# Optimization experiments

Measured on AMD Instinct MI355X. Metric: run time of the kernel, lower is better.

The kernel has to match this reference:

```python
import jax, jax.numpy as jnp
import numpy as np

DIM = 384
HEADS = 8
HD = DIM // HEADS          # 48
RES = 7
N = RES * RES              # 49
B = 2048
SCALE = HD ** (-0.5)
EPS = 1e-12                # torch F.normalize default eps


def setup_inputs() -> dict:
    key = jax.random.key(0)
    ks = jax.random.split(key, 16)
    w = lambda k, shape: jax.random.normal(k, shape, jnp.float32) * 0.02
    return {
        "x": jax.random.normal(ks[0], (B, RES, RES, DIM), jnp.float32),
        # 1x1 convs stored as [out_ch, in_ch]
        "Wq": w(ks[1], (DIM, DIM)), "bq": w(ks[2], (DIM,)),
        "Wk": w(ks[3], (DIM, DIM)), "bk": w(ks[4], (DIM,)),
        "Wv": w(ks[5], (DIM, DIM)), "bv": w(ks[6], (DIM,)),
        # depthwise 3x3 conv, HWIO layout with feature_group_count=DIM -> [3,3,1,DIM]
        "Wvl": w(ks[7], (3, 3, 1, DIM)), "bvl": w(ks[8], (DIM,)),
        # talking-head 1x1 convs over the head axis: [out_heads, in_heads]
        "Wth1": w(ks[9], (HEADS, HEADS)), "bth1": w(ks[10], (HEADS,)),
        "Wth2": w(ks[11], (HEADS, HEADS)), "bth2": w(ks[12], (HEADS,)),
        "Wp": w(ks[13], (DIM, DIM)), "bp": w(ks[14], (DIM,)),
    }


def _conv1x1(x, W, b):
    # x: [B,H,W,C]; W: [O,C]
    return jnp.einsum('bhwc,oc->bhwo', x, W) + b


def _split_heads(y):
    # [B,H,W,DIM] -> [B, heads, head_dim, N]
    b = y.shape[0]
    return y.reshape(b, N, HEADS, HD).transpose(0, 2, 3, 1)


def _l2norm(t):
    # normalize over last axis (spatial N), matching F.normalize(dim=-1)
    n = jnp.sqrt(jnp.sum(t * t, axis=-1, keepdims=True))
    return t / jnp.maximum(n, EPS)


def reference(x, Wq, bq, Wk, bk, Wv, bv, Wvl, bvl,
              Wth1, bth1, Wth2, bth2, Wp, bp):
    # x: [B, H, W, C] (module internally permutes to NCHW; we stay NHWC)
    Bc, H, W_, C = x.shape
    q = _l2norm(_split_heads(_conv1x1(x, Wq, bq)))   # [B,h,c,N]
    k = _l2norm(_split_heads(_conv1x1(x, Wk, bk)))   # [B,h,c,N]
    v_map = _conv1x1(x, Wv, bv)                      # [B,H,W,DIM]
    v_local = jax.lax.conv_general_dilated(
        v_map, Wvl, window_strides=(1, 1), padding='SAME',
        dimension_numbers=('NHWC', 'HWIO', 'NHWC'),
        feature_group_count=DIM) + bvl               # depthwise 3x3
    v = _split_heads(v_map)                          # [B,h,c,N]

    # channel-channel attention: [B, heads, c, c]
    attn = jnp.einsum('bhcn,bhdn->bhcd', q, k) * SCALE
    attn = jnp.einsum('bhcd,gh->bgcd', attn, Wth1) + bth1[None, :, None, None]
    attn = jax.nn.softmax(attn, axis=-1)
    attn = jnp.einsum('bhcd,gh->bgcd', attn, Wth2) + bth2[None, :, None, None]

    o = jnp.einsum('bhcd,bhdn->bhcn', attn, v)       # [B,h,c,N]
    o = o.transpose(0, 3, 1, 2).reshape(Bc, H, W_, DIM) + v_local
    o = _conv1x1(jax.nn.relu(o), Wp, bp)
    return o
```

## Files before the change

kernel.cpp:

```cpp
#include <hip/hip_runtime.h>
#include <hip/hip_bf16.h>


typedef __attribute__((ext_vector_type(8))) short short8;
typedef __attribute__((ext_vector_type(4))) short short4v;
typedef __attribute__((ext_vector_type(4))) float f32x4;

#define NPOS   49
#define DIMC   384
#define SCALE_QK 0.14433756729740643f

#define REGA 0
#define REGB 38416
#define WOFF 36864
#define LDS_BYTES 76832

#define WBLK 159744

__device__ __forceinline__ unsigned short f2bf(float f) {
  __hip_bfloat16 h = __float2bfloat16(f);
  unsigned short u;
  __builtin_memcpy(&u, &h, 2);
  return u;
}
__device__ __forceinline__ float bf2f(unsigned short u) {
  union { unsigned u; float f; } v; v.u = ((unsigned)u) << 16;
  return v.f;
}

__global__ void wconv_kernel(const float* __restrict__ Wq, const float* __restrict__ Wk,
                             const float* __restrict__ Wv, const float* __restrict__ Wp,
                             const float* __restrict__ bq, const float* __restrict__ bk,
                             const float* __restrict__ bv, const float* __restrict__ bp,
                             unsigned short* __restrict__ dst) {
  int t = blockIdx.x * 256 + threadIdx.x;
  if (t >= 79872) return;
  int l = t & 63;
  int u = t >> 6;
  int ks = u % 13; u /= 13;
  int nt = u % 24;
  int g  = u / 24;
  const float* W  = (g == 0) ? Wq : (g == 1) ? Wk : (g == 2) ? Wv : Wp;
  const float* bb = (g == 0) ? bq : (g == 1) ? bk : (g == 2) ? bv : bp;
  int row = nt * 16 + (l & 15);
  short8 o8 = {0,0,0,0,0,0,0,0};
  if (ks < 12) {
    const float* sp = W + row * 384 + ks * 32 + (l >> 4) * 8;
    #pragma unroll
    for (int j = 0; j < 8; ++j) o8[j] = (short)f2bf(sp[j]);
  } else if ((l >> 4) == 0) {
    o8[0] = (short)f2bf(bb[row]);
  }
  *(short8*)(dst + (size_t)t * 8) = o8;
}

__device__ __forceinline__ void xpose_n(const f32x4 (&acc)[4],
                                        int lhi, int llo,
                                        short8 (&fr)[2], float& sc) {
  float ss = 0.f;
  #pragma unroll
  for (int m = 0; m < 4; ++m)
    #pragma unroll
    for (int r = 0; r < 4; ++r) {
      int np = m * 16 + lhi * 4 + r;
      float v = acc[m][r];
      if (np < 49) ss += v * v;
    }
  ss += __shfl_xor(ss, 16, 64);
  ss += __shfl_xor(ss, 32, 64);
  sc = 1.f / fmaxf(sqrtf(ss), 1e-12f);
  const int src_lo = llo + ((lhi & 1) << 5);
  const int src_hi = src_lo + 16;
  #pragma unroll
  for (int m = 0; m < 4; ++m) {
    unsigned p0 = (unsigned)f2bf(acc[m][0]) | ((unsigned)f2bf(acc[m][1]) << 16);
    unsigned p1 = (unsigned)f2bf(acc[m][2]) | ((unsigned)f2bf(acc[m][3]) << 16);
    int lo0 = __shfl((int)p0, src_lo, 64);
    int lo1 = __shfl((int)p1, src_lo, 64);
    int hi0 = __shfl((int)p0, src_hi, 64);
    int hi1 = __shfl((int)p1, src_hi, 64);
    if ((lhi >> 1) == (m & 1)) {
      union { int i[4]; short8 s; } u;
      u.i[0] = lo0; u.i[1] = lo1; u.i[2] = hi0; u.i[3] = hi1;
      fr[m >> 1] = u.s;
    }
  }
  if (lhi == 2) {
    union { int i[4]; short8 s; } u; u.s = fr[1];
    u.i[0] &= 0xFFFF; u.i[1] = 0; u.i[2] = 0; u.i[3] = 0;
    fr[1] = u.s;
  } else if (lhi == 3) {
    short8 z = {0,0,0,0,0,0,0,0};
    fr[1] = z;
  }
}

__global__ __launch_bounds__(512, 4) void attn_fused_kernel(
    const float* __restrict__ x,
    const float* __restrict__ Wvl, const float* __restrict__ bvl,
    const float* __restrict__ Wth1, const float* __restrict__ bth1,
    const float* __restrict__ Wth2, const float* __restrict__ bth2,
    const unsigned short* __restrict__ Wbf,
    float* __restrict__ out) {
  extern __shared__ char smem[];
  const int tid = threadIdx.x;
  const int l   = tid & 63;
  const int w   = tid >> 6;
  const int lhi = l >> 4;
  const int llo = l & 15;
  const int b   = blockIdx.x;

  const float* xb = x + (size_t)b * (NPOS * DIMC);
  const unsigned short* Wq_p = Wbf;
  const unsigned short* Wk_p = Wbf + WBLK;
  const unsigned short* Wv_p = Wbf + 2 * WBLK;
  const unsigned short* Wp_p = Wbf + 3 * WBLK;

  for (int idx = tid; idx < 49 * 48; idx += 512) {
    int row = idx / 48, c8 = idx % 48;
    const float4 v0 = *(const float4*)(xb + row * 384 + c8 * 8);
    const float4 v1 = *(const float4*)(xb + row * 384 + c8 * 8 + 4);
    short8 s;
    s[0] = (short)f2bf(v0.x); s[1] = (short)f2bf(v0.y);
    s[2] = (short)f2bf(v0.z); s[3] = (short)f2bf(v0.w);
    s[4] = (short)f2bf(v1.x); s[5] = (short)f2bf(v1.y);
    s[6] = (short)f2bf(v1.z); s[7] = (short)f2bf(v1.w);
    *(short8*)(smem + REGA + row * 784 + c8 * 16) = s;
  }
  if (tid < 49) {
    short8 u1 = {0,0,0,0,0,0,0,0};
    u1[0] = (short)f2bf(1.0f);
    *(short8*)(smem + REGA + tid * 784 + 768) = u1;
  }
  if (tid >= 64 && tid < 68) {
    short8 z = {0,0,0,0,0,0,0,0};
    *(short8*)(smem + REGB + (tid - 64) * 16) = z;
  }
  __syncthreads();

  short8 qfv[3][2], kfv[3][2];
  float  qscv[3], kscv[3];

#define FENCE asm volatile("" ::: "memory")
#define GEMM_N(WPTR, NIDX, ACC)                                                \
  {                                                                            \
    for (int ks = 0; ks < 13; ++ks) {                                          \
      short8 a[4];                                                             \
      _Pragma("unroll")                                                        \
      for (int m = 0; m < 4; ++m) {                                            \
        int row = m * 16 + llo; row = (row > 48) ? 48 : row;                   \
        a[m] = *(const short8*)(smem + REGA + row * 784 + ks * 64 + lhi * 16); \
      }                                                                        \
      short8 b8 = *(const short8*)(WPTR + (((w * 3 + NIDX) * 13 + ks) << 9) + (l << 3)); \
      _Pragma("unroll")                                                        \
      for (int m = 0; m < 4; ++m)                                              \
        ACC[m] = __builtin_amdgcn_mfma_f32_16x16x32_bf16(a[m], b8, ACC[m], 0, 0, 0); \
    }                                                                          \
  }

  #pragma unroll
  for (int n = 0; n < 3; ++n) {
    f32x4 aV[4] = {};
    GEMM_N(Wv_p, n, aV);
    const int o = (w * 3 + n) * 16 + llo;
    #pragma unroll
    for (int m = 0; m < 4; ++m)
      #pragma unroll
      for (int r = 0; r < 4; ++r) {
        int np = m * 16 + lhi * 4 + r;
        if (np < 49)
          *(unsigned short*)(smem + REGB + np * 784 + o * 2) = f2bf(aV[m][r]);
      }
    FENCE;
  }

  {
    { f32x4 acc[4] = {}; GEMM_N(Wq_p, 0, acc); xpose_n(acc, lhi, llo, qfv[0], qscv[0]); FENCE; }
    { f32x4 acc[4] = {}; GEMM_N(Wq_p, 1, acc); xpose_n(acc, lhi, llo, qfv[1], qscv[1]); FENCE; }
    { f32x4 acc[4] = {}; GEMM_N(Wq_p, 2, acc); xpose_n(acc, lhi, llo, qfv[2], qscv[2]); FENCE; }
  }
  {
    { f32x4 acc[4] = {}; GEMM_N(Wk_p, 0, acc); xpose_n(acc, lhi, llo, kfv[0], kscv[0]); FENCE; }
    { f32x4 acc[4] = {}; GEMM_N(Wk_p, 1, acc); xpose_n(acc, lhi, llo, kfv[1], kscv[1]); FENCE; }
    { f32x4 acc[4] = {}; GEMM_N(Wk_p, 2, acc); xpose_n(acc, lhi, llo, kfv[2], kscv[2]); FENCE; }
  }

  f32x4 g[3][3] = {};
  #pragma unroll
  for (int ks = 0; ks < 2; ++ks)
    #pragma unroll
    for (int mt = 0; mt < 3; ++mt)
      #pragma unroll
      for (int dt = 0; dt < 3; ++dt)
        g[mt][dt] = __builtin_amdgcn_mfma_f32_16x16x32_bf16(qfv[mt][ks], kfv[dt][ks], g[mt][dt], 0, 0, 0);

  float invQv[3][4];
  #pragma unroll
  for (int mt = 0; mt < 3; ++mt)
    #pragma unroll
    for (int r = 0; r < 4; ++r)
      invQv[mt][r] = __shfl(qscv[mt], lhi * 4 + r, 64);

  __syncthreads();

  #pragma unroll
  for (int mt = 0; mt < 3; ++mt)
    #pragma unroll
    for (int dt = 0; dt < 3; ++dt)
      #pragma unroll
      for (int r = 0; r < 4; ++r) {
        int c = mt * 16 + lhi * 4 + r, d = dt * 16 + llo;
        float val = g[mt][dt][r] * invQv[mt][r] * kscv[dt];
        *(unsigned short*)(smem + REGA + ((w * 48 + c) * 48 + d) * 2) = f2bf(val);
      }
  if (tid < 64)       *(float*)(smem + WOFF + tid * 4) = Wth1[tid] * SCALE_QK;
  else if (tid < 72)  *(float*)(smem + WOFF + 256 + (tid - 64) * 4) = bth1[tid - 64];
  else if (tid < 136) *(float*)(smem + WOFF + 288 + (tid - 72) * 4) = Wth2[tid - 72];
  else if (tid < 144) *(float*)(smem + WOFF + 544 + (tid - 136) * 4) = bth2[tid - 136];
  __syncthreads();

  for (int s = tid; s < 2304; s += 512) {
    char* base = smem + REGA + s * 2;
    float gg[8];
    #pragma unroll
    for (int hh = 0; hh < 8; ++hh) gg[hh] = bf2f(*(unsigned short*)(base + hh * 4608));
    #pragma unroll
    for (int gdx = 0; gdx < 8; ++gdx) {
      float t = *(const float*)(smem + WOFF + 256 + gdx * 4);
      #pragma unroll
      for (int hh = 0; hh < 8; ++hh)
        t += gg[hh] * *(const float*)(smem + WOFF + (gdx * 8 + hh) * 4);
      *(unsigned short*)(base + gdx * 4608) = f2bf(t);
    }
  }
  __syncthreads();

  for (int row = tid; row < 384; row += 512) {
    char* rp = smem + REGA + row * 96;
    float vv[48];
    #pragma unroll
    for (int i = 0; i < 6; ++i) {
      short8 v8 = *(short8*)(rp + i * 16);
      #pragma unroll
      for (int j = 0; j < 8; ++j) vv[i * 8 + j] = bf2f((unsigned short)v8[j]);
    }
    float mx = vv[0];
    #pragma unroll
    for (int i = 1; i < 48; ++i) mx = fmaxf(mx, vv[i]);
    float sum = 0.f;
    #pragma unroll
    for (int i = 0; i < 48; ++i) { vv[i] = __expf(vv[i] - mx); sum += vv[i]; }
    float inv = 1.f / sum;
    #pragma unroll
    for (int i = 0; i < 6; ++i) {
      short8 o8;
      #pragma unroll
      for (int j = 0; j < 8; ++j) o8[j] = (short)f2bf(vv[i * 8 + j] * inv);
      *(short8*)(rp + i * 16) = o8;
    }
  }
  __syncthreads();

  for (int s = tid; s < 2304; s += 512) {
    char* base = smem + REGA + s * 2;
    float gg[8];
    #pragma unroll
    for (int hh = 0; hh < 8; ++hh) gg[hh] = bf2f(*(unsigned short*)(base + hh * 4608));
    #pragma unroll
    for (int gdx = 0; gdx < 8; ++gdx) {
      float t = *(const float*)(smem + WOFF + 544 + gdx * 4);
      #pragma unroll
      for (int hh = 0; hh < 8; ++hh)
        t += gg[hh] * *(const float*)(smem + WOFF + 288 + (gdx * 8 + hh) * 4);
      *(unsigned short*)(base + gdx * 4608) = f2bf(t);
    }
  }
  __syncthreads();

  f32x4 oacc[3][4] = {};
  {
    #pragma unroll
    for (int ks = 0; ks < 2; ++ks) {
      short8 af[3];
      #pragma unroll
      for (int m = 0; m < 3; ++m) {
        short8 t = {0,0,0,0,0,0,0,0};
        if (!(ks == 1 && lhi >= 2))
          t = *(const short8*)(smem + REGA + (w * 48 + m * 16 + llo) * 96 + ks * 64 + lhi * 16);
        af[m] = t;
      }
      #pragma unroll
      for (int nt = 0; nt < 4; ++nt) {
        int n = nt * 16 + llo; int nc = (n > 48) ? 48 : n;
        short8 bf8 = {0,0,0,0,0,0,0,0};
        if (!(ks == 1 && lhi >= 2))
          bf8 = *(const short8*)(smem + REGB + nc * 784 + w * 96 + ks * 64 + lhi * 16);
        #pragma unroll
        for (int m = 0; m < 3; ++m)
          oacc[m][nt] = __builtin_amdgcn_mfma_f32_16x16x32_bf16(af[m], bf8, oacc[m][nt], 0, 0, 0);
      }
    }
  }
  __syncthreads();

  #pragma unroll
  for (int m = 0; m < 3; ++m)
    #pragma unroll
    for (int nt = 0; nt < 4; ++nt) {
      const int n = nt * 16 + llo;
      if (n >= 49) continue;
      const int o0 = w * 48 + m * 16 + lhi * 4;
      short4v ot;
      #pragma unroll
      for (int r = 0; r < 4; ++r) ot[r] = (short)f2bf(oacc[m][nt][r]);
      *(short4v*)(smem + REGA + n * 784 + o0 * 2) = ot;
    }
  __syncthreads();

  for (int idx = tid; idx < 2352; idx += 512) {
    int n = idx / 48, c8 = idx % 48;
    int o0 = c8 * 8;
    int y = n / 7, xq = n % 7;
    float a[8];
    #pragma unroll
    for (int j = 0; j < 8; ++j) a[j] = bvl[o0 + j];
    #pragma unroll
    for (int dy = 0; dy < 3; ++dy) {
      int yy = y + dy - 1;
      if (yy < 0 || yy > 6) continue;
      #pragma unroll
      for (int dx = 0; dx < 3; ++dx) {
        int xx = xq + dx - 1;
        if (xx < 0 || xx > 6) continue;
        short8 vv = *(const short8*)(smem + REGB + (yy * 7 + xx) * 784 + o0 * 2);
        const float* wp = Wvl + (dy * 3 + dx) * 384 + o0;
        #pragma unroll
        for (int j = 0; j < 8; ++j) a[j] += bf2f((unsigned short)vv[j]) * wp[j];
      }
    }
    char* p = smem + REGA + n * 784 + o0 * 2;
    short8 oc = *(short8*)p;
    short8 s8;
    #pragma unroll
    for (int j = 0; j < 8; ++j)
      s8[j] = (short)f2bf(fmaxf(bf2f((unsigned short)oc[j]) + a[j], 0.f));
    *(short8*)p = s8;
  }
  if (tid < 49) {
    short8 u1 = {0,0,0,0,0,0,0,0};
    u1[0] = (short)f2bf(1.0f);
    *(short8*)(smem + REGA + tid * 784 + 768) = u1;
  }
  __syncthreads();

  {
    f32x4 acc[4][3] = {};
    for (int ks = 0; ks < 13; ++ks) {
      short8 a[4];
      #pragma unroll
      for (int m = 0; m < 4; ++m) {
        int row = m * 16 + llo; row = (row > 48) ? 48 : row;
        a[m] = *(const short8*)(smem + REGA + row * 784 + ks * 64 + lhi * 16);
      }
      #pragma unroll
      for (int n = 0; n < 3; ++n) {
        const int nt = w * 3 + n;
        short8 bfr = *(const short8*)(Wp_p + ((nt * 13 + ks) << 9) + (l << 3));
        #pragma unroll
        for (int m = 0; m < 4; ++m)
          acc[m][n] = __builtin_amdgcn_mfma_f32_16x16x32_bf16(a[m], bfr, acc[m][n], 0, 0, 0);
      }
    }
    float* ob = out + (size_t)b * (NPOS * DIMC);
    #pragma unroll
    for (int n = 0; n < 3; ++n) {
      const int o = (w * 3 + n) * 16 + llo;
      #pragma unroll
      for (int m = 0; m < 4; ++m)
        #pragma unroll
        for (int r = 0; r < 4; ++r) {
          int np = m * 16 + lhi * 4 + r;
          if (np < 49) ob[np * 384 + o] = acc[m][n][r];
        }
    }
  }
}

extern "C" void kernel_launch(void* const* d_in, const int* in_sizes, int n_in,
                              void* d_out, int out_size, void* d_ws, size_t ws_size,
                              hipStream_t stream) {
  const float* x    = (const float*)d_in[0];
  const float* Wq   = (const float*)d_in[1];
  const float* bq   = (const float*)d_in[2];
  const float* Wk   = (const float*)d_in[3];
  const float* bk   = (const float*)d_in[4];
  const float* Wv   = (const float*)d_in[5];
  const float* bv   = (const float*)d_in[6];
  const float* Wvl  = (const float*)d_in[7];
  const float* bvl  = (const float*)d_in[8];
  const float* Wth1 = (const float*)d_in[9];
  const float* bth1 = (const float*)d_in[10];
  const float* Wth2 = (const float*)d_in[11];
  const float* bth2 = (const float*)d_in[12];
  const float* Wp   = (const float*)d_in[13];
  const float* bp   = (const float*)d_in[14];
  unsigned short* Wbf = (unsigned short*)d_ws;
  float* out = (float*)d_out;

  hipLaunchKernelGGL(wconv_kernel, dim3(312), dim3(256), 0, stream,
                     Wq, Wk, Wv, Wp, bq, bk, bv, bp, Wbf);
  hipLaunchKernelGGL(attn_fused_kernel, dim3(2048), dim3(512), LDS_BYTES, stream,
                     x, Wvl, bvl, Wth1, bth1, Wth2, bth2, Wbf, out);
}
```

Measured before the change: 292.9 us.

## Keep talking-head mixing and softmax in registers with head-interleaved swizzled LDS layout

Stores attention scores in LDS with all 8 heads interleaved per (c,d) site and an XOR swizzle. Each wave can then read the 8-head vector in one load and compute the talking-head mix for its own output head in registers. Softmax now runs in registers with cross-lane shuffles instead of a separate LDS pass. The second head mix feeds straight into the MFMA A-fragments via an in-register transpose, which removes a round trip through LDS. This cuts several LDS passes and barriers, but adds more register pressure under launch bounds of 512 threads with 4 blocks.

```diff
diff --git a/kernel.cpp b/kernel.cpp
--- a/kernel.cpp
+++ b/kernel.cpp
@@ -12,7 +12,6 @@
 
 #define REGA 0
 #define REGB 38416
-#define WOFF 36864
 #define LDS_BYTES 76832
 
 #define WBLK 159744
@@ -26,6 +25,10 @@
 __device__ __forceinline__ float bf2f(unsigned short u) {
   union { unsigned u; float f; } v; v.u = ((unsigned)u) << 16;
   return v.f;
+}
+
+__device__ __forceinline__ int site_off(int c, int d) {
+  return (c * 48 + (d ^ (c & 7))) << 4;
 }
 
 __global__ void wconv_kernel(const float* __restrict__ Wq, const float* __restrict__ Wk,
@@ -54,21 +57,8 @@
   *(short8*)(dst + (size_t)t * 8) = o8;
 }
 
-__device__ __forceinline__ void xpose_n(const f32x4 (&acc)[4],
-                                        int lhi, int llo,
-                                        short8 (&fr)[2], float& sc) {
-  float ss = 0.f;
-  #pragma unroll
-  for (int m = 0; m < 4; ++m)
-    #pragma unroll
-    for (int r = 0; r < 4; ++r) {
-      int np = m * 16 + lhi * 4 + r;
-      float v = acc[m][r];
-      if (np < 49) ss += v * v;
-    }
-  ss += __shfl_xor(ss, 16, 64);
-  ss += __shfl_xor(ss, 32, 64);
-  sc = 1.f / fmaxf(sqrtf(ss), 1e-12f);
+__device__ __forceinline__ void xpose_core(const f32x4 (&acc)[4],
+                                           int lhi, int llo, short8 (&fr)[2]) {
   const int src_lo = llo + ((lhi & 1) << 5);
   const int src_hi = src_lo + 16;
   #pragma unroll
@@ -85,6 +75,24 @@
       fr[m >> 1] = u.s;
     }
   }
+}
+
+__device__ __forceinline__ void xpose_n(const f32x4 (&acc)[4],
+                                        int lhi, int llo,
+                                        short8 (&fr)[2], float& sc) {
+  float ss = 0.f;
+  #pragma unroll
+  for (int m = 0; m < 4; ++m)
+    #pragma unroll
+    for (int r = 0; r < 4; ++r) {
+      int np = m * 16 + lhi * 4 + r;
+      float v = acc[m][r];
+      if (np < 49) ss += v * v;
+    }
+  ss += __shfl_xor(ss, 16, 64);
+  ss += __shfl_xor(ss, 32, 64);
+  sc = 1.f / fmaxf(sqrtf(ss), 1e-12f);
+  xpose_core(acc, lhi, llo, fr);
   if (lhi == 2) {
     union { int i[4]; short8 s; } u; u.s = fr[1];
     u.i[0] &= 0xFFFF; u.i[1] = 0; u.i[2] = 0; u.i[3] = 0;
@@ -115,6 +123,15 @@
   const unsigned short* Wk_p = Wbf + WBLK;
   const unsigned short* Wv_p = Wbf + 2 * WBLK;
   const unsigned short* Wp_p = Wbf + 3 * WBLK;
+
+  float w1r[8], w2r[8];
+  #pragma unroll
+  for (int h = 0; h < 8; ++h) {
+    w1r[h] = Wth1[w * 8 + h] * SCALE_QK;
+    w2r[h] = Wth2[w * 8 + h];
+  }
+  const float b1s = bth1[w];
+  const float b2s = bth2[w];
 
   for (int idx = tid; idx < 49 * 48; idx += 512) {
     int row = idx / 48, c8 = idx % 48;
@@ -174,16 +191,12 @@
     FENCE;
   }
 
-  {
-    { f32x4 acc[4] = {}; GEMM_N(Wq_p, 0, acc); xpose_n(acc, lhi, llo, qfv[0], qscv[0]); FENCE; }
-    { f32x4 acc[4] = {}; GEMM_N(Wq_p, 1, acc); xpose_n(acc, lhi, llo, qfv[1], qscv[1]); FENCE; }
-    { f32x4 acc[4] = {}; GEMM_N(Wq_p, 2, acc); xpose_n(acc, lhi, llo, qfv[2], qscv[2]); FENCE; }
-  }
-  {
-    { f32x4 acc[4] = {}; GEMM_N(Wk_p, 0, acc); xpose_n(acc, lhi, llo, kfv[0], kscv[0]); FENCE; }
-    { f32x4 acc[4] = {}; GEMM_N(Wk_p, 1, acc); xpose_n(acc, lhi, llo, kfv[1], kscv[1]); FENCE; }
-    { f32x4 acc[4] = {}; GEMM_N(Wk_p, 2, acc); xpose_n(acc, lhi, llo, kfv[2], kscv[2]); FENCE; }
-  }
+  { f32x4 acc[4] = {}; GEMM_N(Wq_p, 0, acc); xpose_n(acc, lhi, llo, qfv[0], qscv[0]); FENCE; }
+  { f32x4 acc[4] = {}; GEMM_N(Wq_p, 1, acc); xpose_n(acc, lhi, llo, qfv[1], qscv[1]); FENCE; }
+  { f32x4 acc[4] = {}; GEMM_N(Wq_p, 2, acc); xpose_n(acc, lhi, llo, qfv[2], qscv[2]); FENCE; }
+  { f32x4 acc[4] = {}; GEMM_N(Wk_p, 0, acc); xpose_n(acc, lhi, llo, kfv[0], kscv[0]); FENCE; }
+  { f32x4 acc[4] = {}; GEMM_N(Wk_p, 1, acc); xpose_n(acc, lhi, llo, kfv[1], kscv[1]); FENCE; }
+  { f32x4 acc[4] = {}; GEMM_N(Wk_p, 2, acc); xpose_n(acc, lhi, llo, kfv[2], kscv[2]); FENCE; }
 
   f32x4 g[3][3] = {};
   #pragma unroll
@@ -211,108 +224,98 @@
       for (int r = 0; r < 4; ++r) {
         int c = mt * 16 + lhi * 4 + r, d = dt * 16 + llo;
         float val = g[mt][dt][r] * invQv[mt][r] * kscv[dt];
-        *(unsigned short*)(smem + REGA + ((w * 48 + c) * 48 + d) * 2) = f2bf(val);
-      }
-  if (tid < 64)       *(float*)(smem + WOFF + tid * 4) = Wth1[tid] * SCALE_QK;
-  else if (tid < 72)  *(float*)(smem + WOFF + 256 + (tid - 64) * 4) = bth1[tid - 64];
-  else if (tid < 136) *(float*)(smem + WOFF + 288 + (tid - 72) * 4) = Wth2[tid - 72];
-  else if (tid < 144) *(float*)(smem + WOFF + 544 + (tid - 136) * 4) = bth2[tid - 136];
-  __syncthreads();
-
-  for (int s = tid; s < 2304; s += 512) {
-    char* base = smem + REGA + s * 2;
-    float gg[8];
-    #pragma unroll
-    for (int hh = 0; hh < 8; ++hh) gg[hh] = bf2f(*(unsigned short*)(base + hh * 4608));
-    #pragma unroll
-    for (int gdx = 0; gdx < 8; ++gdx) {
-      float t = *(const float*)(smem + WOFF + 256 + gdx * 4);
-      #pragma unroll
-      for (int hh = 0; hh < 8; ++hh)
-        t += gg[hh] * *(const float*)(smem + WOFF + (gdx * 8 + hh) * 4);
-      *(unsigned short*)(base + gdx * 4608) = f2bf(t);
-    }
-  }
-  __syncthreads();
-
-  for (int row = tid; row < 384; row += 512) {
-    char* rp = smem + REGA + row * 96;
-    float vv[48];
-    #pragma unroll
-    for (int i = 0; i < 6; ++i) {
-      short8 v8 = *(short8*)(rp + i * 16);
-      #pragma unroll
-      for (int j = 0; j < 8; ++j) vv[i * 8 + j] = bf2f((unsigned short)v8[j]);
-    }
-    float mx = vv[0];
-    #pragma unroll
-    for (int i = 1; i < 48; ++i) mx = fmaxf(mx, vv[i]);
-    float sum = 0.f;
-    #pragma unroll
-    for (int i = 0; i < 48; ++i) { vv[i] = __expf(vv[i] - mx); sum += vv[i]; }
-    float inv = 1.f / sum;
-    #pragma unroll
-    for (int i = 0; i < 6; ++i) {
-      short8 o8;
-      #pragma unroll
-      for (int j = 0; j < 8; ++j) o8[j] = (short)f2bf(vv[i * 8 + j] * inv);
-      *(short8*)(rp + i * 16) = o8;
-    }
-  }
-  __syncthreads();
-
-  for (int s = tid; s < 2304; s += 512) {
-    char* base = smem + REGA + s * 2;
-    float gg[8];
-    #pragma unroll
-    for (int hh = 0; hh < 8; ++hh) gg[hh] = bf2f(*(unsigned short*)(base + hh * 4608));
-    #pragma unroll
-    for (int gdx = 0; gdx < 8; ++gdx) {
-      float t = *(const float*)(smem + WOFF + 544 + gdx * 4);
-      #pragma unroll
-      for (int hh = 0; hh < 8; ++hh)
-        t += gg[hh] * *(const float*)(smem + WOFF + 288 + (gdx * 8 + hh) * 4);
-      *(unsigned short*)(base + gdx * 4608) = f2bf(t);
-    }
-  }
-  __syncthreads();
+        *(unsigned short*)(smem + REGA + site_off(c, d) + 2 * w) = f2bf(val);
+      }
+  __syncthreads();
+
+  f32x4 p1[3][3];
+  #pragma unroll
+  for (int mt = 0; mt < 3; ++mt)
+    #pragma unroll
+    for (int dt = 0; dt < 3; ++dt)
+      #pragma unroll
+      for (int r = 0; r < 4; ++r) {
+        int c = mt * 16 + lhi * 4 + r, d = dt * 16 + llo;
+        short8 hv = *(const short8*)(smem + REGA + site_off(c, d));
+        float t = b1s;
+        #pragma unroll
+        for (int h = 0; h < 8; ++h) t += bf2f((unsigned short)hv[h]) * w1r[h];
+        p1[mt][dt][r] = t;
+      }
+  #pragma unroll
+  for (int mt = 0; mt < 3; ++mt)
+    #pragma unroll
+    for (int r = 0; r < 4; ++r) {
+      float mx = fmaxf(fmaxf(p1[mt][0][r], p1[mt][1][r]), p1[mt][2][r]);
+      #pragma unroll
+      for (int msk = 1; msk < 16; msk <<= 1) mx = fmaxf(mx, __shfl_xor(mx, msk, 64));
+      float e0 = __expf(p1[mt][0][r] - mx);
+      float e1 = __expf(p1[mt][1][r] - mx);
+      float e2 = __expf(p1[mt][2][r] - mx);
+      float s = e0 + e1 + e2;
+      #pragma unroll
+      for (int msk = 1; msk < 16; msk <<= 1) s += __shfl_xor(s, msk, 64);
+      float inv = 1.f / s;
+      p1[mt][0][r] = e0 * inv; p1[mt][1][r] = e1 * inv; p1[mt][2][r] = e2 * inv;
+    }
+  __syncthreads();
+
+  #pragma unroll
+  for (int mt = 0; mt < 3; ++mt)
+    #pragma unroll
+    for (int dt = 0; dt < 3; ++dt)
+      #pragma unroll
+      for (int r = 0; r < 4; ++r) {
+        int c = mt * 16 + lhi * 4 + r, d = dt * 16 + llo;
+        *(unsigned short*)(smem + REGA + site_off(c, d) + 2 * w) = f2bf(p1[mt][dt][r]);
+      }
+  __syncthreads();
+
+  short8 attf[3][2];
+  #pragma unroll
+  for (int ct = 0; ct < 3; ++ct) {
+    f32x4 in2[4];
+    in2[3] = (f32x4){0.f, 0.f, 0.f, 0.f};
+    #pragma unroll
+    for (int m = 0; m < 3; ++m)
+      #pragma unroll
+      for (int r = 0; r < 4; ++r) {
+        int c2 = ct * 16 + llo;
+        int d2 = m * 16 + lhi * 4 + r;
+        short8 pv = *(const short8*)(smem + REGA + site_off(c2, d2));
+        float t = b2s;
+        #pragma unroll
+        for (int h = 0; h < 8; ++h) t += bf2f((unsigned short)pv[h]) * w2r[h];
+        in2[m][r] = t;
+      }
+    xpose_core(in2, lhi, llo, attf[ct]);
+  }
 
   f32x4 oacc[3][4] = {};
-  {
-    #pragma unroll
-    for (int ks = 0; ks < 2; ++ks) {
-      short8 af[3];
-      #pragma unroll
-      for (int m = 0; m < 3; ++m) {
-        short8 t = {0,0,0,0,0,0,0,0};
-        if (!(ks == 1 && lhi >= 2))
-          t = *(const short8*)(smem + REGA + (w * 48 + m * 16 + llo) * 96 + ks * 64 + lhi * 16);
-        af[m] = t;
-      }
-      #pragma unroll
-      for (int nt = 0; nt < 4; ++nt) {
-        int n = nt * 16 + llo; int nc = (n > 48) ? 48 : n;
-        short8 bf8 = {0,0,0,0,0,0,0,0};
-        if (!(ks == 1 && lhi >= 2))
-          bf8 = *(const short8*)(smem + REGB + nc * 784 + w * 96 + ks * 64 + lhi * 16);
-        #pragma unroll
-        for (int m = 0; m < 3; ++m)
-          oacc[m][nt] = __builtin_amdgcn_mfma_f32_16x16x32_bf16(af[m], bf8, oacc[m][nt], 0, 0, 0);
-      }
-    }
-  }
-  __syncthreads();
-
-  #pragma unroll
-  for (int m = 0; m < 3; ++m)
+  #pragma unroll
+  for (int ks = 0; ks < 2; ++ks)
+    #pragma unroll
+    for (int nt = 0; nt < 4; ++nt) {
+      int n = nt * 16 + llo; int nc = (n > 48) ? 48 : n;
+      short8 bf8 = {0,0,0,0,0,0,0,0};
+      if (!(ks == 1 && lhi >= 2))
+        bf8 = *(const short8*)(smem + REGB + nc * 784 + w * 96 + ks * 64 + lhi * 16);
+      #pragma unroll
+      for (int ct = 0; ct < 3; ++ct)
+        oacc[ct][nt] = __builtin_amdgcn_mfma_f32_16x16x32_bf16(attf[ct][ks], bf8, oacc[ct][nt], 0, 0, 0);
+    }
+  __syncthreads();
+
+  #pragma unroll
+  for (int ct = 0; ct < 3; ++ct)
     #pragma unroll
     for (int nt = 0; nt < 4; ++nt) {
       const int n = nt * 16 + llo;
       if (n >= 49) continue;
-      const int o0 = w * 48 + m * 16 + lhi * 4;
+      const int o0 = w * 48 + ct * 16 + lhi * 4;
       short4v ot;
       #pragma unroll
-      for (int r = 0; r < 4; ++r) ot[r] = (short)f2bf(oacc[m][nt][r]);
+      for (int r = 0; r < 4; ++r) ot[r] = (short)f2bf(oacc[ct][nt][r]);
       *(short4v*)(smem + REGA + n * 784 + o0 * 2) = ot;
     }
   __syncthreads();
```

Result: slower. 349.9 us (+19.5%).
